# Kernel tuning notes

Measured on AMD Instinct MI355X. Metric: run time of the kernel, lower is better.

## Reference

```python
import jax, jax.numpy as jnp
import numpy as np

B = 8192
D_IN = 10
H = 1900


def _l2norm_cols(w):
    # tf.nn.l2_normalize(w, dim=0): normalize each column, eps 1e-12
    sq = jnp.sum(w * w, axis=0, keepdims=True)
    return w * jax.lax.rsqrt(jnp.maximum(sq, 1e-12))


def setup_inputs() -> dict:
    key = jax.random.key(0)
    ks = jax.random.split(key, 12)
    return {
        "inputs": jax.random.normal(ks[0], (B, D_IN), jnp.float32),
        "c_prev": jax.random.normal(ks[1], (B, H), jnp.float32),
        "h_prev": jax.random.normal(ks[2], (B, H), jnp.float32),
        "wx": jax.random.normal(ks[3], (D_IN, 4 * H), jnp.float32) * 0.1,
        "wh": jax.random.normal(ks[4], (H, 4 * H), jnp.float32) * 0.1,
        "wmx": jax.random.normal(ks[5], (D_IN, H), jnp.float32) * 0.1,
        "wmh": jax.random.normal(ks[6], (H, H), jnp.float32) * 0.1,
        "b": jax.random.normal(ks[7], (4 * H,), jnp.float32) * 0.1,
        "gx": jax.random.uniform(ks[8], (4 * H,), jnp.float32, 0.5, 1.5),
        "gh": jax.random.uniform(ks[9], (4 * H,), jnp.float32, 0.5, 1.5),
        "gmx": jax.random.uniform(ks[10], (H,), jnp.float32, 0.5, 1.5),
        "gmh": jax.random.uniform(ks[11], (H,), jnp.float32, 0.5, 1.5),
    }


def reference(inputs, c_prev, h_prev, wx, wh, wmx, wmh, b, gx, gh, gmx, gmh):
    # weight-normalized weights (per-column l2 norm * gain)
    wx_n = _l2norm_cols(wx) * gx
    wh_n = _l2norm_cols(wh) * gh
    wmx_n = _l2norm_cols(wmx) * gmx
    wmh_n = _l2norm_cols(wmh) * gmh
    # multiplicative state m: [B, H]
    m = (inputs @ wmx_n) * (h_prev @ wmh_n)
    # gate pre-activations z: [B, 4H]
    z = inputs @ wx_n + m @ wh_n + b
    i, f, o, u = jnp.split(z, 4, axis=1)
    i = jax.nn.sigmoid(i)
    f = jax.nn.sigmoid(f)
    o = jax.nn.sigmoid(o)
    u = jnp.tanh(u)
    c = f * c_prev + i * u
    h = o * jnp.tanh(c)
    return (h, c)
```

## Files before the change

### kernel.cpp

```cpp
#include <hip/hip_runtime.h>

typedef unsigned short ushort_t;
typedef short bf16x8 __attribute__((ext_vector_type(8)));
typedef float f32x4 __attribute__((ext_vector_type(4)));

#define H 1900
#define FH 7600
#define BATCH 8192
#define KP 1952
#define NP_A 1920
#define NB 7680
#define BK 32
#define KITERS (KP / BK)

static const size_t OFF_SWX  = 0;
static const size_t OFF_SWH  = 32768;
static const size_t OFF_SWMX = 65536;
static const size_t OFF_SWMH = 73728;
static const size_t OFF_WMXN = 81920;
static const size_t OFF_PART = 163840;
static const size_t OFF_HBF  = 786432;
static const size_t OFF_MEXT = OFF_HBF + 31981568;
static const size_t OFF_WMHT = OFF_MEXT + 31981568;
static const size_t OFF_WHXT = OFF_WMHT + 7495680;

#define PW_X  0
#define PW_H  60800
#define PW_MX 121600
#define PW_MH 136800

__device__ __forceinline__ ushort_t f2bf(float x) {
  unsigned u = __float_as_uint(x);
  return (ushort_t)((u + 0x7fffu + ((u >> 16) & 1u)) >> 16);
}

__device__ __forceinline__ void gl_lds16(const ushort_t* g, ushort_t* lds) {
  __builtin_amdgcn_global_load_lds(
      (const __attribute__((address_space(1))) unsigned int*)(g),
      (__attribute__((address_space(3))) unsigned int*)(lds), 16, 0, 0);
}

__global__ void colsum_partial_kernel(const float* __restrict__ wx, const float* __restrict__ wh,
                                      const float* __restrict__ wmx, const float* __restrict__ wmh,
                                      float* __restrict__ parts) {
  int c = blockIdx.x * 256 + threadIdx.x;
  int y = blockIdx.y, p = blockIdx.z;
  const float* W; int K, N; float* out;
  if (y == 0)      { W = wx;  K = 10;   N = FH; out = parts + PW_X  + (size_t)p * FH; }
  else if (y == 1) { W = wh;  K = 1900; N = FH; out = parts + PW_H  + (size_t)p * FH; }
  else if (y == 2) { W = wmx; K = 10;   N = H;  out = parts + PW_MX + (size_t)p * H;  }
  else             { W = wmh; K = 1900; N = H;  out = parts + PW_MH + (size_t)p * H;  }
  if (c >= N) return;
  int rp = (K + 7) / 8;
  int r0 = p * rp, r1 = r0 + rp; if (r1 > K) r1 = K;
  float s = 0.f;
  for (int r = r0; r < r1; ++r) { float v = W[(size_t)r * N + c]; s += v * v; }
  out[c] = s;
}

__global__ void scales_final_kernel(const float* __restrict__ parts,
                                    const float* __restrict__ gx, const float* __restrict__ gh,
                                    const float* __restrict__ gmx, const float* __restrict__ gmh,
                                    float* __restrict__ s_wx, float* __restrict__ s_wh,
                                    float* __restrict__ s_wmx, float* __restrict__ s_wmh) {
  int c = blockIdx.x * 256 + threadIdx.x;
  int y = blockIdx.y;
  const float* pp; int N; const float* g; float* out;
  if (y == 0)      { pp = parts + PW_X;  N = FH; g = gx;  out = s_wx;  }
  else if (y == 1) { pp = parts + PW_H;  N = FH; g = gh;  out = s_wh;  }
  else if (y == 2) { pp = parts + PW_MX; N = H;  g = gmx; out = s_wmx; }
  else             { pp = parts + PW_MH; N = H;  g = gmh; out = s_wmh; }
  if (c >= N) return;
  float s = 0.f;
  for (int p = 0; p < 8; ++p) s += pp[(size_t)p * N + c];
  out[c] = g[c] * rsqrtf(fmaxf(s, 1e-12f));
}

__global__ void cvt_h_kernel(const float* __restrict__ h_prev, ushort_t* __restrict__ hbf) {
  size_t idx = (size_t)blockIdx.x * 256 + threadIdx.x;
  int row = (int)(idx / KP), col = (int)(idx % KP);
  float v = (col < H) ? h_prev[(size_t)row * H + col] : 0.f;
  hbf[idx] = f2bf(v);
}

__global__ void wmxn_kernel(const float* __restrict__ wmx, const float* __restrict__ s_wmx,
                            float* __restrict__ wmxn) {
  int idx = blockIdx.x * 256 + threadIdx.x;
  int i = idx / NP_A, j = idx - i * NP_A;
  wmxn[idx] = (j < H) ? wmx[i * H + j] * s_wmx[j] : 0.f;
}

__global__ void wmhT_kernel(const float* __restrict__ wmh, const float* __restrict__ s_wmh,
                            ushort_t* __restrict__ wmhT) {
  __shared__ float tile[32][33];
  int n0 = blockIdx.x * 32, k0 = blockIdx.y * 32;
  int tx = threadIdx.x & 31, ty = threadIdx.x >> 5;
#pragma unroll
  for (int it = 0; it < 4; ++it) {
    int k = k0 + ty + it * 8, n = n0 + tx;
    float v = (k < H && n < H) ? wmh[(size_t)k * H + n] : 0.f;
    tile[ty + it * 8][tx] = v;
  }
  __syncthreads();
#pragma unroll
  for (int it = 0; it < 4; ++it) {
    int n = n0 + ty + it * 8, k = k0 + tx;
    float v = tile[tx][ty + it * 8];
    float s = (n < H) ? s_wmh[n] : 0.f;
    wmhT[(size_t)n * KP + k] = f2bf(v * s);
  }
}

__global__ void whxT_kernel(const float* __restrict__ wh, const float* __restrict__ wx,
                            const float* __restrict__ s_wh, const float* __restrict__ s_wx,
                            ushort_t* __restrict__ whxT) {
  __shared__ float tile[32][33];
  int c0 = blockIdx.x * 32, k0 = blockIdx.y * 32;
  int tx = threadIdx.x & 31, ty = threadIdx.x >> 5;
#pragma unroll
  for (int it = 0; it < 4; ++it) {
    int k = k0 + ty + it * 8, c = c0 + tx;
    float v = 0.f;
    if (c < FH) {
      if (k < H) v = wh[(size_t)k * FH + c] * s_wh[c];
      else if (k >= NP_A && k < NP_A + 10) v = wx[(size_t)(k - NP_A) * FH + c] * s_wx[c];
    }
    tile[ty + it * 8][tx] = v;
  }
  __syncthreads();
#pragma unroll
  for (int it = 0; it < 4; ++it) {
    int c = c0 + ty + it * 8, k = k0 + tx;
    if (c < FH) {
      int g = c / H; int j = c - g * H; int n = 4 * j + g;
      whxT[(size_t)n * KP + k] = f2bf(tile[tx][ty + it * 8]);
    }
  }
}

__global__ void mext_tail_kernel(const float* __restrict__ inputs, ushort_t* __restrict__ m_ext) {
  int idx = blockIdx.x * 256 + threadIdx.x;
  int row = idx >> 5, c = idx & 31;
  float v = (c < 10) ? inputs[(size_t)row * 10 + c] : 0.f;
  m_ext[(size_t)row * KP + NP_A + c] = f2bf(v);
}

__global__ void whxT_tail_kernel(ushort_t* __restrict__ whxT) {
  int idx = blockIdx.x * 256 + threadIdx.x;
  whxT[(size_t)FH * KP + idx] = 0;
}

__device__ __forceinline__ void gemm_tile(const ushort_t* __restrict__ Ag,
                                          const ushort_t* __restrict__ Bg,
                                          int m0, int n0,
                                          ushort_t* As, ushort_t* Bs,
                                          f32x4 acc[4][4]) {
  const int tid = threadIdx.x;
  const int lane = tid & 63;
  const int quad = lane >> 4;
  const int lo = lane & 15;
  const int wave = tid >> 6;
  const int wm = (wave & 1) << 6;
  const int wn = (wave >> 1) << 6;
  const int sw = (lo >> 1) & 3;

  const int cr = lane >> 2;
  const int hg = (lane & 3) ^ ((lane >> 3) & 3);
  const int r0 = wave * 16 + cr;
  const int r1 = 64 + wave * 16 + cr;
  const ushort_t* gA0 = Ag + (size_t)(m0 + r0) * KP + hg * 8;
  const ushort_t* gA1 = Ag + (size_t)(m0 + r1) * KP + hg * 8;
  const ushort_t* gB0 = Bg + (size_t)(n0 + r0) * KP + hg * 8;
  const ushort_t* gB1 = Bg + (size_t)(n0 + r1) * KP + hg * 8;
  ushort_t* lA0 = As + (wave * 16) * BK;
  ushort_t* lA1 = As + (64 + wave * 16) * BK;
  ushort_t* lB0 = Bs + (wave * 16) * BK;
  ushort_t* lB1 = Bs + (64 + wave * 16) * BK;

  for (int kt = 0; kt < KITERS; ++kt) {
    __syncthreads();
    gl_lds16(gA0, lA0);
    gl_lds16(gA1, lA1);
    gl_lds16(gB0, lB0);
    gl_lds16(gB1, lB1);
    __syncthreads();
    bf16x8 af[4], bfv[4];
#pragma unroll
    for (int mf = 0; mf < 4; ++mf)
      af[mf] = *(const bf16x8*)(As + (wm + mf * 16 + lo) * BK + ((quad ^ sw) << 3));
#pragma unroll
    for (int nf = 0; nf < 4; ++nf)
      bfv[nf] = *(const bf16x8*)(Bs + (wn + nf * 16 + lo) * BK + ((quad ^ sw) << 3));
#pragma unroll
    for (int mf = 0; mf < 4; ++mf)
#pragma unroll
      for (int nf = 0; nf < 4; ++nf)
        acc[mf][nf] = __builtin_amdgcn_mfma_f32_16x16x32_bf16(af[mf], bfv[nf], acc[mf][nf], 0, 0, 0);
    gA0 += BK; gA1 += BK; gB0 += BK; gB1 += BK;
  }
}

__global__ void __launch_bounds__(256) gemmA_kernel(const ushort_t* __restrict__ hbf,
                                                    const ushort_t* __restrict__ wmhT,
                                                    const float* __restrict__ inputs,
                                                    const float* __restrict__ wmxn,
                                                    ushort_t* __restrict__ m_ext) {
  __shared__ __align__(16) char smem[16384];
  ushort_t* As = (ushort_t*)smem;
  ushort_t* Bs = (ushort_t*)(smem + 8192);
  f32x4 acc[4][4];
  f32x4 zv = {0.f, 0.f, 0.f, 0.f};
#pragma unroll
  for (int a = 0; a < 4; ++a)
#pragma unroll
    for (int bq = 0; bq < 4; ++bq) acc[a][bq] = zv;
  int m0 = blockIdx.x * 128, n0 = blockIdx.y * 128;
  gemm_tile(hbf, wmhT, m0, n0, As, Bs, acc);
  __syncthreads();
  float* inL  = (float*)smem;
  float* wmxL = (float*)(smem + 5120);
  for (int t = threadIdx.x; t < 1280; t += 256) {
    int r = t / 10, i = t - r * 10;
    inL[t] = inputs[(size_t)(m0 + r) * 10 + i];
  }
  for (int t = threadIdx.x; t < 1280; t += 256) {
    int i = t >> 7, c = t & 127;
    wmxL[t] = wmxn[i * NP_A + n0 + c];
  }
  __syncthreads();
  const int lane = threadIdx.x & 63, quad = lane >> 4, lo = lane & 15;
  const int wave = threadIdx.x >> 6, wm = (wave & 1) << 6, wn = (wave >> 1) << 6;
#pragma unroll
  for (int mf = 0; mf < 4; ++mf)
#pragma unroll
    for (int r = 0; r < 4; ++r) {
      int rl = wm + mf * 16 + quad * 4 + r;
      float inrow[10];
#pragma unroll
      for (int i = 0; i < 10; ++i) inrow[i] = inL[rl * 10 + i];
#pragma unroll
      for (int nf = 0; nf < 4; ++nf) {
        int cl = wn + nf * 16 + lo;
        float mx = 0.f;
#pragma unroll
        for (int i = 0; i < 10; ++i) mx += inrow[i] * wmxL[i * 128 + cl];
        float mv = acc[mf][nf][r] * mx;
        m_ext[(size_t)(m0 + rl) * KP + (n0 + cl)] = f2bf(mv);
      }
    }
}

__global__ void __launch_bounds__(256) gemmB_kernel(const ushort_t* __restrict__ mext,
                                                    const ushort_t* __restrict__ whxT,
                                                    const float* __restrict__ bvec,
                                                    const float* __restrict__ c_prev,
                                                    float* __restrict__ hout,
                                                    float* __restrict__ cout) {
  __shared__ __align__(16) char smem[16384];
  ushort_t* As = (ushort_t*)smem;
  ushort_t* Bs = (ushort_t*)(smem + 8192);
  f32x4 acc[4][4];
  f32x4 zv = {0.f, 0.f, 0.f, 0.f};
#pragma unroll
  for (int a = 0; a < 4; ++a)
#pragma unroll
    for (int bq = 0; bq < 4; ++bq) acc[a][bq] = zv;
  int m0 = blockIdx.x * 128, n0 = blockIdx.y * 128;
  gemm_tile(mext, whxT, m0, n0, As, Bs, acc);
  const int lane = threadIdx.x & 63, quad = lane >> 4, lo = lane & 15;
  const int wave = threadIdx.x >> 6, wm = (wave & 1) << 6, wn = (wave >> 1) << 6;
#pragma unroll
  for (int nf = 0; nf < 4; ++nf) {
    int gn = n0 + wn + nf * 16 + lo;
    int j = gn >> 2, g = gn & 3;
    float bias = (j < H) ? bvec[g * H + j] : 0.f;
#pragma unroll
    for (int mf = 0; mf < 4; ++mf)
#pragma unroll
      for (int r = 0; r < 4; ++r) {
        float zs = acc[mf][nf][r] + bias;
        float v1 = __shfl_xor(zs, 1);
        float v2 = __shfl_xor(zs, 2);
        float v3 = __shfl_xor(v1, 2);
        if (g == r && j < H) {
          float zi, zf, zo, zu;
          { int t = 0 ^ g; zi = t == 0 ? zs : t == 1 ? v1 : t == 2 ? v2 : v3; }
          { int t = 1 ^ g; zf = t == 0 ? zs : t == 1 ? v1 : t == 2 ? v2 : v3; }
          { int t = 2 ^ g; zo = t == 0 ? zs : t == 1 ? v1 : t == 2 ? v2 : v3; }
          { int t = 3 ^ g; zu = t == 0 ? zs : t == 1 ? v1 : t == 2 ? v2 : v3; }
          float iv = 1.f / (1.f + __expf(-zi));
          float fv = 1.f / (1.f + __expf(-zf));
          float ov = 1.f / (1.f + __expf(-zo));
          float uv = tanhf(zu);
          int row = m0 + wm + mf * 16 + quad * 4 + r;
          size_t oidx = (size_t)row * H + j;
          float cp = c_prev[oidx];
          float cv = fv * cp + iv * uv;
          hout[oidx] = ov * tanhf(cv);
          cout[oidx] = cv;
        }
      }
  }
}

extern "C" void kernel_launch(void* const* d_in, const int* in_sizes, int n_in,
                              void* d_out, int out_size, void* d_ws, size_t ws_size,
                              hipStream_t stream) {
  const float* inputs = (const float*)d_in[0];
  const float* c_prev = (const float*)d_in[1];
  const float* h_prev = (const float*)d_in[2];
  const float* wx  = (const float*)d_in[3];
  const float* wh  = (const float*)d_in[4];
  const float* wmx = (const float*)d_in[5];
  const float* wmh = (const float*)d_in[6];
  const float* bv  = (const float*)d_in[7];
  const float* gx  = (const float*)d_in[8];
  const float* gh  = (const float*)d_in[9];
  const float* gmx = (const float*)d_in[10];
  const float* gmh = (const float*)d_in[11];

  char* ws = (char*)d_ws;
  float* s_wx  = (float*)(ws + OFF_SWX);
  float* s_wh  = (float*)(ws + OFF_SWH);
  float* s_wmx = (float*)(ws + OFF_SWMX);
  float* s_wmh = (float*)(ws + OFF_SWMH);
  float* wmxn  = (float*)(ws + OFF_WMXN);
  float* parts = (float*)(ws + OFF_PART);
  ushort_t* hbf   = (ushort_t*)(ws + OFF_HBF);
  ushort_t* m_ext = (ushort_t*)(ws + OFF_MEXT);
  ushort_t* wmhT  = (ushort_t*)(ws + OFF_WMHT);
  ushort_t* whxT  = (ushort_t*)(ws + OFF_WHXT);

  float* hout = (float*)d_out;
  float* cout = hout + (size_t)BATCH * H;

  colsum_partial_kernel<<<dim3(30, 4, 8), 256, 0, stream>>>(wx, wh, wmx, wmh, parts);
  scales_final_kernel<<<dim3(30, 4), 256, 0, stream>>>(parts, gx, gh, gmx, gmh,
                                                       s_wx, s_wh, s_wmx, s_wmh);
  cvt_h_kernel<<<62464, 256, 0, stream>>>(h_prev, hbf);
  wmxn_kernel<<<75, 256, 0, stream>>>(wmx, s_wmx, wmxn);
  wmhT_kernel<<<dim3(60, 61), 256, 0, stream>>>(wmh, s_wmh, wmhT);
  whxT_kernel<<<dim3(238, 61), 256, 0, stream>>>(wh, wx, s_wh, s_wx, whxT);
  mext_tail_kernel<<<1024, 256, 0, stream>>>(inputs, m_ext);
  whxT_tail_kernel<<<610, 256, 0, stream>>>(whxT);
  gemmA_kernel<<<dim3(64, 15), 256, 0, stream>>>(hbf, wmhT, inputs, wmxn, m_ext);
  gemmB_kernel<<<dim3(64, 60), 256, 0, stream>>>(m_ext, whxT, bv, c_prev, hout, cout);
}
```

Measured before the change: 1.081 ms.

## Double-buffer LDS tiles in GEMM main loop to overlap loads with MFMA

Splits shared memory into two A/B buffers so the next K-slice is loaded into one buffer while MFMAs run on the other. This cuts the K-loop from two barriers per iteration to one and hides global-to-LDS latency. KITERS is odd, so the loop is unrolled by two with a single tail step. LDS per block doubles to 32 KB, which may reduce occupancy.

```diff
diff --git a/kernel.cpp b/kernel.cpp
--- a/kernel.cpp
+++ b/kernel.cpp
@@ -12,6 +12,7 @@
 #define NB 7680
 #define BK 32
 #define KITERS (KP / BK)
+static_assert(KITERS % 2 == 1, "tail handling assumes odd KITERS");
 
 static const size_t OFF_SWX  = 0;
 static const size_t OFF_SWH  = 32768;
@@ -150,11 +151,45 @@
   whxT[(size_t)FH * KP + idx] = 0;
 }
 
+
+__device__ __forceinline__ void mfma_step(const ushort_t* As, const ushort_t* Bs,
+                                          int wm, int wn, int lo, int quad, int sw,
+                                          f32x4 acc[4][4]) {
+  bf16x8 af[4], bfv[4];
+#pragma unroll
+  for (int mf = 0; mf < 4; ++mf)
+    af[mf] = *(const bf16x8*)(As + (wm + mf * 16 + lo) * BK + ((quad ^ sw) << 3));
+#pragma unroll
+  for (int nf = 0; nf < 4; ++nf)
+    bfv[nf] = *(const bf16x8*)(Bs + (wn + nf * 16 + lo) * BK + ((quad ^ sw) << 3));
+#pragma unroll
+  for (int mf = 0; mf < 4; ++mf)
+#pragma unroll
+    for (int nf = 0; nf < 4; ++nf)
+      acc[mf][nf] = __builtin_amdgcn_mfma_f32_16x16x32_bf16(af[mf], bfv[nf], acc[mf][nf], 0, 0, 0);
+}
+
+__device__ __forceinline__ void gemm_stage(const ushort_t*& gA0, const ushort_t*& gA1,
+                                           const ushort_t*& gB0, const ushort_t*& gB1,
+                                           ushort_t* lA0, ushort_t* lA1,
+                                           ushort_t* lB0, ushort_t* lB1) {
+  gl_lds16(gA0, lA0);
+  gl_lds16(gA1, lA1);
+  gl_lds16(gB0, lB0);
+  gl_lds16(gB1, lB1);
+  gA0 += BK; gA1 += BK; gB0 += BK; gB1 += BK;
+}
+
 __device__ __forceinline__ void gemm_tile(const ushort_t* __restrict__ Ag,
                                           const ushort_t* __restrict__ Bg,
                                           int m0, int n0,
-                                          ushort_t* As, ushort_t* Bs,
+                                          char* smem,
                                           f32x4 acc[4][4]) {
+  ushort_t* As0 = (ushort_t*)(smem);
+  ushort_t* Bs0 = (ushort_t*)(smem + 8192);
+  ushort_t* As1 = (ushort_t*)(smem + 16384);
+  ushort_t* Bs1 = (ushort_t*)(smem + 24576);
+
   const int tid = threadIdx.x;
   const int lane = tid & 63;
   const int quad = lane >> 4;
@@ -172,32 +207,28 @@
   const ushort_t* gA1 = Ag + (size_t)(m0 + r1) * KP + hg * 8;
   const ushort_t* gB0 = Bg + (size_t)(n0 + r0) * KP + hg * 8;
   const ushort_t* gB1 = Bg + (size_t)(n0 + r1) * KP + hg * 8;
-  ushort_t* lA0 = As + (wave * 16) * BK;
-  ushort_t* lA1 = As + (64 + wave * 16) * BK;
-  ushort_t* lB0 = Bs + (wave * 16) * BK;
-  ushort_t* lB1 = Bs + (64 + wave * 16) * BK;
-
-  for (int kt = 0; kt < KITERS; ++kt) {
+  ushort_t* lA0_0 = As0 + (wave * 16) * BK;
+  ushort_t* lA1_0 = As0 + (64 + wave * 16) * BK;
+  ushort_t* lB0_0 = Bs0 + (wave * 16) * BK;
+  ushort_t* lB1_0 = Bs0 + (64 + wave * 16) * BK;
+  ushort_t* lA0_1 = As1 + (wave * 16) * BK;
+  ushort_t* lA1_1 = As1 + (64 + wave * 16) * BK;
+  ushort_t* lB0_1 = Bs1 + (wave * 16) * BK;
+  ushort_t* lB1_1 = Bs1 + (64 + wave * 16) * BK;
+
+  gemm_stage(gA0, gA1, gB0, gB1, lA0_0, lA1_0, lB0_0, lB1_0);
+  __syncthreads();
+
+  for (int kt = 0; kt + 2 < KITERS; kt += 2) {
+    gemm_stage(gA0, gA1, gB0, gB1, lA0_1, lA1_1, lB0_1, lB1_1);
+    mfma_step(As0, Bs0, wm, wn, lo, quad, sw, acc);
     __syncthreads();
-    gl_lds16(gA0, lA0);
-    gl_lds16(gA1, lA1);
-    gl_lds16(gB0, lB0);
-    gl_lds16(gB1, lB1);
+    gemm_stage(gA0, gA1, gB0, gB1, lA0_0, lA1_0, lB0_0, lB1_0);
+    mfma_step(As1, Bs1, wm, wn, lo, quad, sw, acc);
     __syncthreads();
-    bf16x8 af[4], bfv[4];
-#pragma unroll
-    for (int mf = 0; mf < 4; ++mf)
-      af[mf] = *(const bf16x8*)(As + (wm + mf * 16 + lo) * BK + ((quad ^ sw) << 3));
-#pragma unroll
-    for (int nf = 0; nf < 4; ++nf)
-      bfv[nf] = *(const bf16x8*)(Bs + (wn + nf * 16 + lo) * BK + ((quad ^ sw) << 3));
-#pragma unroll
-    for (int mf = 0; mf < 4; ++mf)
-#pragma unroll
-      for (int nf = 0; nf < 4; ++nf)
-        acc[mf][nf] = __builtin_amdgcn_mfma_f32_16x16x32_bf16(af[mf], bfv[nf], acc[mf][nf], 0, 0, 0);
-    gA0 += BK; gA1 += BK; gB0 += BK; gB1 += BK;
-  }
+  }
+  mfma_step(As0, Bs0, wm, wn, lo, quad, sw, acc);
+  __syncthreads();
 }
 
 __global__ void __launch_bounds__(256) gemmA_kernel(const ushort_t* __restrict__ hbf,
@@ -205,9 +236,7 @@
                                                     const float* __restrict__ inputs,
                                                     const float* __restrict__ wmxn,
                                                     ushort_t* __restrict__ m_ext) {
-  __shared__ __align__(16) char smem[16384];
-  ushort_t* As = (ushort_t*)smem;
-  ushort_t* Bs = (ushort_t*)(smem + 8192);
+  __shared__ __align__(16) char smem[32768];
   f32x4 acc[4][4];
   f32x4 zv = {0.f, 0.f, 0.f, 0.f};
 #pragma unroll
@@ -215,8 +244,7 @@
 #pragma unroll
     for (int bq = 0; bq < 4; ++bq) acc[a][bq] = zv;
   int m0 = blockIdx.x * 128, n0 = blockIdx.y * 128;
-  gemm_tile(hbf, wmhT, m0, n0, As, Bs, acc);
-  __syncthreads();
+  gemm_tile(hbf, wmhT, m0, n0, smem, acc);
   float* inL  = (float*)smem;
   float* wmxL = (float*)(smem + 5120);
   for (int t = threadIdx.x; t < 1280; t += 256) {
@@ -256,9 +284,7 @@
                                                     const float* __restrict__ c_prev,
                                                     float* __restrict__ hout,
                                                     float* __restrict__ cout) {
-  __shared__ __align__(16) char smem[16384];
-  ushort_t* As = (ushort_t*)smem;
-  ushort_t* Bs = (ushort_t*)(smem + 8192);
+  __shared__ __align__(16) char smem[32768];
   f32x4 acc[4][4];
   f32x4 zv = {0.f, 0.f, 0.f, 0.f};
 #pragma unroll
@@ -266,7 +292,7 @@
 #pragma unroll
     for (int bq = 0; bq < 4; ++bq) acc[a][bq] = zv;
   int m0 = blockIdx.x * 128, n0 = blockIdx.y * 128;
-  gemm_tile(mext, whxT, m0, n0, As, Bs, acc);
+  gemm_tile(mext, whxT, m0, n0, smem, acc);
   const int lane = threadIdx.x & 63, quad = lane >> 4, lo = lane & 15;
   const int wave = threadIdx.x >> 6, wm = (wave & 1) << 6, wn = (wave >> 1) << 6;
 #pragma unroll
```

After: 1.239 ms. 1.15x slower.

## Replace gate GEMM with 256x256 double-buffered 8-wave pipelined kernel

Applied to the files above, without the earlier changes.

The second GEMM (m_ext × whxT with fused LSTM epilogue) moves from 128x128 tiles with 256 threads to 256x256 tiles with 512 threads. It uses 128KB of dynamic LDS split into two buffers, and global-to-LDS loads for the next K-steps are interleaved with MFMA quarter-tiles. Barriers, setprio and explicit vmcnt waits pace that interleave, and a block-index swizzle groups tiles for L2 reuse. The aim is to raise arithmetic intensity and hide load latency in the dominant GEMM. In exchange it adds heavy register pressure from 128 accumulators per thread and a K tail handled as a separate step, and only one block fits per CU because of the LDS size.

```diff
diff --git a/kernel.cpp b/kernel.cpp
--- a/kernel.cpp
+++ b/kernel.cpp
@@ -12,6 +12,8 @@
 #define NB 7680
 #define BK 32
 #define KITERS (KP / BK)
+
+#define NKT 30
 
 static const size_t OFF_SWX  = 0;
 static const size_t OFF_SWH  = 32768;
@@ -28,6 +30,12 @@
 #define PW_H  60800
 #define PW_MX 121600
 #define PW_MH 136800
+
+#define BAR() __builtin_amdgcn_s_barrier()
+#define PRIO1 __builtin_amdgcn_s_setprio(1)
+#define PRIO0 __builtin_amdgcn_s_setprio(0)
+#define WAIT_LGKM0 asm volatile("s_waitcnt lgkmcnt(0)" ::: "memory")
+#define WAIT_VM(N) asm volatile("s_waitcnt vmcnt(" #N ")" ::: "memory")
 
 __device__ __forceinline__ ushort_t f2bf(float x) {
   unsigned u = __float_as_uint(x);
@@ -150,11 +158,11 @@
   whxT[(size_t)FH * KP + idx] = 0;
 }
 
-__device__ __forceinline__ void gemm_tile(const ushort_t* __restrict__ Ag,
-                                          const ushort_t* __restrict__ Bg,
-                                          int m0, int n0,
-                                          ushort_t* As, ushort_t* Bs,
-                                          f32x4 acc[4][4]) {
+__device__ __forceinline__ void gemm_tile128(const ushort_t* __restrict__ Ag,
+                                             const ushort_t* __restrict__ Bg,
+                                             int m0, int n0,
+                                             ushort_t* As, ushort_t* Bs,
+                                             f32x4 acc[4][4]) {
   const int tid = threadIdx.x;
   const int lane = tid & 63;
   const int quad = lane >> 4;
@@ -215,7 +223,7 @@
 #pragma unroll
     for (int bq = 0; bq < 4; ++bq) acc[a][bq] = zv;
   int m0 = blockIdx.x * 128, n0 = blockIdx.y * 128;
-  gemm_tile(hbf, wmhT, m0, n0, As, Bs, acc);
+  gemm_tile128(hbf, wmhT, m0, n0, As, Bs, acc);
   __syncthreads();
   float* inL  = (float*)smem;
   float* wmxL = (float*)(smem + 5120);
@@ -250,32 +258,182 @@
     }
 }
 
-__global__ void __launch_bounds__(256) gemmB_kernel(const ushort_t* __restrict__ mext,
-                                                    const ushort_t* __restrict__ whxT,
-                                                    const float* __restrict__ bvec,
-                                                    const float* __restrict__ c_prev,
-                                                    float* __restrict__ hout,
-                                                    float* __restrict__ cout) {
-  __shared__ __align__(16) char smem[16384];
-  ushort_t* As = (ushort_t*)smem;
-  ushort_t* Bs = (ushort_t*)(smem + 8192);
-  f32x4 acc[4][4];
+
+__device__ __forceinline__ void stage_half(const ushort_t* __restrict__ G, int Rg, int kb,
+                                           ushort_t* L, int tid) {
+  const int wave = tid >> 6;
+#pragma unroll
+  for (int q = 0; q < 2; ++q) {
+    const int idx = q * 512 + tid;
+    const int r = idx >> 3, s = idx & 7;
+    const int gs = s ^ (r & 7);
+    gl_lds16(G + (size_t)(Rg + r) * KP + kb + gs * 8,
+             L + (size_t)(q * 512 + wave * 64) * 8);
+  }
+}
+
+__device__ __forceinline__ void read_Ahalf(const ushort_t* A, int wmL, int lo, int mh,
+                                           int sw0, int sw1, bf16x8 af[8]) {
+#pragma unroll
+  for (int mf = 0; mf < 4; ++mf) {
+    const ushort_t* p = A + ((wmL + mh * 64 + mf * 16 + lo) << 6);
+    af[mf * 2 + 0] = *(const bf16x8*)(p + sw0);
+    af[mf * 2 + 1] = *(const bf16x8*)(p + sw1);
+  }
+}
+
+__device__ __forceinline__ void read_Bhalf(const ushort_t* B, int wnL, int lo, int nh,
+                                           int sw0, int sw1, bf16x8 bf[4]) {
+#pragma unroll
+  for (int nf = 0; nf < 2; ++nf) {
+    const ushort_t* p = B + ((wnL + nh * 32 + nf * 16 + lo) << 6);
+    bf[nf * 2 + 0] = *(const bf16x8*)(p + sw0);
+    bf[nf * 2 + 1] = *(const bf16x8*)(p + sw1);
+  }
+}
+
+__device__ __forceinline__ void mfma_quad(const bf16x8 af[8], const bf16x8 bf[4],
+                                          f32x4 acc[8][4], int mh, int nh) {
+#pragma unroll
+  for (int mf = 0; mf < 4; ++mf)
+#pragma unroll
+    for (int nf = 0; nf < 2; ++nf) {
+      f32x4 c = acc[mh * 4 + mf][nh * 2 + nf];
+      c = __builtin_amdgcn_mfma_f32_16x16x32_bf16(af[mf * 2 + 0], bf[nf * 2 + 0], c, 0, 0, 0);
+      c = __builtin_amdgcn_mfma_f32_16x16x32_bf16(af[mf * 2 + 1], bf[nf * 2 + 1], c, 0, 0, 0);
+      acc[mh * 4 + mf][nh * 2 + nf] = c;
+    }
+}
+
+template <int MODE>
+__device__ __forceinline__ void b8_iter(const ushort_t* __restrict__ Ag,
+                                        const ushort_t* __restrict__ Bg,
+                                        int m0, int n0, int T,
+                                        ushort_t* Acur, ushort_t* Bcur,
+                                        ushort_t* Anxt, ushort_t* Bnxt,
+                                        int tid, int lo, int wmL, int wnL,
+                                        int sw0, int sw1, f32x4 acc[8][4]) {
+  bf16x8 af[8], b0f[4], b1f[4];
+  read_Ahalf(Acur, wmL, lo, 0, sw0, sw1, af);
+  read_Bhalf(Bcur, wnL, lo, 0, sw0, sw1, b0f);
+  if (MODE <= 1) stage_half(Ag, m0 + 128, (T + 1) * 64, Anxt + 8192, tid);
+  BAR(); WAIT_LGKM0;
+  PRIO1; mfma_quad(af, b0f, acc, 0, 0); PRIO0;
+  BAR();
+  read_Bhalf(Bcur, wnL, lo, 1, sw0, sw1, b1f);
+  BAR(); WAIT_LGKM0;
+  PRIO1; mfma_quad(af, b1f, acc, 0, 1); PRIO0;
+  BAR();
+  read_Ahalf(Acur, wmL, lo, 1, sw0, sw1, af);
+  if (MODE == 0) stage_half(Bg, n0, (T + 2) * 64, Bcur, tid);
+  BAR(); WAIT_LGKM0;
+  PRIO1; mfma_quad(af, b1f, acc, 1, 1); PRIO0;
+  BAR();
+  if (MODE == 0) {
+    stage_half(Ag, m0, (T + 2) * 64, Acur, tid);
+    stage_half(Bg, n0 + 128, (T + 2) * 64, Bcur + 8192, tid);
+    WAIT_VM(6);
+  } else if (MODE == 1) {
+    WAIT_VM(0);
+  }
+  BAR();
+  PRIO1; mfma_quad(af, b0f, acc, 1, 0); PRIO0;
+  BAR();
+}
+
+__global__ void __launch_bounds__(512, 2)
+gemmB8_kernel(const ushort_t* __restrict__ mext, const ushort_t* __restrict__ whxT,
+              const float* __restrict__ bvec, const float* __restrict__ c_prev,
+              float* __restrict__ hout, float* __restrict__ cout) {
+  extern __shared__ __align__(16) char smem[];
+  ushort_t* As0 = (ushort_t*)smem;
+  ushort_t* Bs0 = (ushort_t*)(smem + 32768);
+  ushort_t* As1 = (ushort_t*)(smem + 65536);
+  ushort_t* Bs1 = (ushort_t*)(smem + 98304);
+
+  const int tid = threadIdx.x;
+  const int lane = tid & 63;
+  const int lo = lane & 15, quad = lane >> 4;
+  const int wave = tid >> 6;
+  const int wmL = (wave & 1) << 7;
+  const int wnL = (wave >> 1) << 6;
+  const int sw0 = ((quad ^ (lo & 7)) << 3);
+  const int sw1 = (((4 | quad) ^ (lo & 7)) << 3);
+
+  int bid = blockIdx.x;
+  int swz = (bid & 7) * 120 + (bid >> 3);
+  int mt = swz & 31, nt = swz >> 5;
+  int m0 = mt << 8, n0 = nt << 8;
+
+  f32x4 acc[8][4];
   f32x4 zv = {0.f, 0.f, 0.f, 0.f};
 #pragma unroll
-  for (int a = 0; a < 4; ++a)
+  for (int a = 0; a < 8; ++a)
 #pragma unroll
     for (int bq = 0; bq < 4; ++bq) acc[a][bq] = zv;
-  int m0 = blockIdx.x * 128, n0 = blockIdx.y * 128;
-  gemm_tile(mext, whxT, m0, n0, As, Bs, acc);
-  const int lane = threadIdx.x & 63, quad = lane >> 4, lo = lane & 15;
-  const int wave = threadIdx.x >> 6, wm = (wave & 1) << 6, wn = (wave >> 1) << 6;
+
+  const ushort_t* Ag = mext;
+  const ushort_t* Bg = whxT;
+
+  stage_half(Ag, m0,       0,  As0,        tid);
+  stage_half(Bg, n0,       0,  Bs0,        tid);
+  stage_half(Ag, m0 + 128, 0,  As0 + 8192, tid);
+  stage_half(Bg, n0 + 128, 0,  Bs0 + 8192, tid);
+  stage_half(Bg, n0,       64, Bs1,        tid);
+  stage_half(Ag, m0,       64, As1,        tid);
+  stage_half(Bg, n0 + 128, 64, Bs1 + 8192, tid);
+  WAIT_VM(6);
+  BAR();
+
+  for (int T = 0; T < NKT - 2; T += 2) {
+    b8_iter<0>(Ag, Bg, m0, n0, T,     As0, Bs0, As1, Bs1, tid, lo, wmL, wnL, sw0, sw1, acc);
+    b8_iter<0>(Ag, Bg, m0, n0, T + 1, As1, Bs1, As0, Bs0, tid, lo, wmL, wnL, sw0, sw1, acc);
+  }
+  b8_iter<1>(Ag, Bg, m0, n0, NKT - 2, As0, Bs0, As1, Bs1, tid, lo, wmL, wnL, sw0, sw1, acc);
+  b8_iter<2>(Ag, Bg, m0, n0, NKT - 1, As1, Bs1, As0, Bs0, tid, lo, wmL, wnL, sw0, sw1, acc);
+
+  {
+    const int wavei = tid >> 6;
+#pragma unroll
+    for (int q = 0; q < 2; ++q) {
+      const int idx = q * 512 + tid;
+      const int r = idx >> 2, s = idx & 3;
+      const int gs = s ^ (r & 3);
+      gl_lds16(Ag + (size_t)(m0 + r) * KP + 1920 + gs * 8,
+               As0 + (size_t)(q * 512 + wavei * 64) * 8);
+    }
+#pragma unroll
+    for (int q = 0; q < 2; ++q) {
+      const int idx = q * 512 + tid;
+      const int r = idx >> 2, s = idx & 3;
+      const int gs = s ^ (r & 3);
+      gl_lds16(Bg + (size_t)(n0 + r) * KP + 1920 + gs * 8,
+               Bs0 + (size_t)(q * 512 + wavei * 64) * 8);
+    }
+    WAIT_VM(0);
+    BAR();
+    const int swt = ((quad ^ (lo & 3)) << 3);
+    bf16x8 a2[8], b2[4];
+#pragma unroll
+    for (int mf = 0; mf < 8; ++mf)
+      a2[mf] = *(const bf16x8*)(As0 + ((wmL + mf * 16 + lo) << 5) + swt);
+#pragma unroll
+    for (int nf = 0; nf < 4; ++nf)
+      b2[nf] = *(const bf16x8*)(Bs0 + ((wnL + nf * 16 + lo) << 5) + swt);
+#pragma unroll
+    for (int mf = 0; mf < 8; ++mf)
+#pragma unroll
+      for (int nf = 0; nf < 4; ++nf)
+        acc[mf][nf] = __builtin_amdgcn_mfma_f32_16x16x32_bf16(a2[mf], b2[nf], acc[mf][nf], 0, 0, 0);
+  }
+
 #pragma unroll
   for (int nf = 0; nf < 4; ++nf) {
-    int gn = n0 + wn + nf * 16 + lo;
+    int gn = n0 + wnL + nf * 16 + lo;
     int j = gn >> 2, g = gn & 3;
     float bias = (j < H) ? bvec[g * H + j] : 0.f;
 #pragma unroll
-    for (int mf = 0; mf < 4; ++mf)
+    for (int mf = 0; mf < 8; ++mf)
 #pragma unroll
       for (int r = 0; r < 4; ++r) {
         float zs = acc[mf][nf][r] + bias;
@@ -292,7 +450,7 @@
           float fv = 1.f / (1.f + __expf(-zf));
           float ov = 1.f / (1.f + __expf(-zo));
           float uv = tanhf(zu);
-          int row = m0 + wm + mf * 16 + quad * 4 + r;
+          int row = m0 + wmL + mf * 16 + quad * 4 + r;
           size_t oidx = (size_t)row * H + j;
           float cp = c_prev[oidx];
           float cv = fv * cp + iv * uv;
@@ -334,6 +492,13 @@
   float* hout = (float*)d_out;
   float* cout = hout + (size_t)BATCH * H;
 
+  static bool attr_set = false;
+  if (!attr_set) {
+    hipFuncSetAttribute(reinterpret_cast<const void*>(&gemmB8_kernel),
+                        hipFuncAttributeMaxDynamicSharedMemorySize, 131072);
+    attr_set = true;
+  }
+
   colsum_partial_kernel<<<dim3(30, 4, 8), 256, 0, stream>>>(wx, wh, wmx, wmh, parts);
   scales_final_kernel<<<dim3(30, 4), 256, 0, stream>>>(parts, gx, gh, gmx, gmh,
                                                        s_wx, s_wh, s_wmx, s_wmh);
@@ -344,5 +509,5 @@
   mext_tail_kernel<<<1024, 256, 0, stream>>>(inputs, m_ext);
   whxT_tail_kernel<<<610, 256, 0, stream>>>(whxT);
   gemmA_kernel<<<dim3(64, 15), 256, 0, stream>>>(hbf, wmhT, inputs, wmxn, m_ext);
-  gemmB_kernel<<<dim3(64, 60), 256, 0, stream>>>(m_ext, whxT, bv, c_prev, hout, cout);
-}
+  gemmB8_kernel<<<dim3(960), 512, 131072, stream>>>(m_ext, whxT, bv, c_prev, hout, cout);
+}
```

After: 1.093 ms. About the same (+1.1%).

## Tile m_ext/whxT into contiguous slabs and triple-buffer gemmB with XCD-aware block mapping

Applied to the files above, without the earlier changes.

Stores m_ext and the transposed gate weights in a 128x32 slab-tiled layout, so each K-step loads one contiguous 8 KB chunk per operand. The main gemm is rewritten as a triple-buffered LDS pipeline that prefetches two slabs ahead using direct global-to-LDS loads, partial vmcnt waits and raw barriers, and raises wave priority around the MFMA block. It also remaps block IDs so each XCD works on a contiguous group of M tiles, aiming for better L2 reuse. The costs are triple the LDS per block (48 KB) and a fragile manual waitcnt schedule.

```diff
diff --git a/kernel.cpp b/kernel.cpp
--- a/kernel.cpp
+++ b/kernel.cpp
@@ -9,9 +9,12 @@
 #define BATCH 8192
 #define KP 1952
 #define NP_A 1920
-#define NB 7680
 #define BK 32
 #define KITERS (KP / BK)
+
+#define NSLAB 61
+#define SLAB_U 4096
+#define PANEL_U 249856
 
 static const size_t OFF_SWX  = 0;
 static const size_t OFF_SWH  = 32768;
@@ -29,6 +32,11 @@
 #define PW_MX 121600
 #define PW_MH 136800
 
+#define BAR() __builtin_amdgcn_s_barrier()
+#define PRIO1 __builtin_amdgcn_s_setprio(1)
+#define PRIO0 __builtin_amdgcn_s_setprio(0)
+#define WAIT_VM(N) asm volatile("s_waitcnt vmcnt(" #N ")" ::: "memory")
+
 __device__ __forceinline__ ushort_t f2bf(float x) {
   unsigned u = __float_as_uint(x);
   return (ushort_t)((u + 0x7fffu + ((u >> 16) & 1u)) >> 16);
@@ -38,6 +46,11 @@
   __builtin_amdgcn_global_load_lds(
       (const __attribute__((address_space(1))) unsigned int*)(g),
       (__attribute__((address_space(3))) unsigned int*)(lds), 16, 0, 0);
+}
+
+__device__ __forceinline__ size_t tiled_addr(int row, int col) {
+  return (size_t)(row >> 7) * PANEL_U + (size_t)(col >> 5) * SLAB_U +
+         (size_t)(row & 127) * 32 + (col & 31);
 }
 
 __global__ void colsum_partial_kernel(const float* __restrict__ wx, const float* __restrict__ wh,
@@ -133,7 +146,7 @@
     int c = c0 + ty + it * 8, k = k0 + tx;
     if (c < FH) {
       int g = c / H; int j = c - g * H; int n = 4 * j + g;
-      whxT[(size_t)n * KP + k] = f2bf(tile[tx][ty + it * 8]);
+      whxT[tiled_addr(n, k)] = f2bf(tile[tx][ty + it * 8]);
     }
   }
 }
@@ -142,19 +155,20 @@
   int idx = blockIdx.x * 256 + threadIdx.x;
   int row = idx >> 5, c = idx & 31;
   float v = (c < 10) ? inputs[(size_t)row * 10 + c] : 0.f;
-  m_ext[(size_t)row * KP + NP_A + c] = f2bf(v);
+  m_ext[tiled_addr(row, 1920 + c)] = f2bf(v);
 }
 
 __global__ void whxT_tail_kernel(ushort_t* __restrict__ whxT) {
   int idx = blockIdx.x * 256 + threadIdx.x;
-  whxT[(size_t)FH * KP + idx] = 0;
-}
-
-__device__ __forceinline__ void gemm_tile(const ushort_t* __restrict__ Ag,
-                                          const ushort_t* __restrict__ Bg,
-                                          int m0, int n0,
-                                          ushort_t* As, ushort_t* Bs,
-                                          f32x4 acc[4][4]) {
+  int n = 7600 + idx / 1952, k = idx % 1952;
+  whxT[tiled_addr(n, k)] = 0;
+}
+
+__device__ __forceinline__ void gemm_tile128(const ushort_t* __restrict__ Ag,
+                                             const ushort_t* __restrict__ Bg,
+                                             int m0, int n0,
+                                             ushort_t* As, ushort_t* Bs,
+                                             f32x4 acc[4][4]) {
   const int tid = threadIdx.x;
   const int lane = tid & 63;
   const int quad = lane >> 4;
@@ -215,7 +229,7 @@
 #pragma unroll
     for (int bq = 0; bq < 4; ++bq) acc[a][bq] = zv;
   int m0 = blockIdx.x * 128, n0 = blockIdx.y * 128;
-  gemm_tile(hbf, wmhT, m0, n0, As, Bs, acc);
+  gemm_tile128(hbf, wmhT, m0, n0, As, Bs, acc);
   __syncthreads();
   float* inL  = (float*)smem;
   float* wmxL = (float*)(smem + 5120);
@@ -245,35 +259,112 @@
 #pragma unroll
         for (int i = 0; i < 10; ++i) mx += inrow[i] * wmxL[i * 128 + cl];
         float mv = acc[mf][nf][r] * mx;
-        m_ext[(size_t)(m0 + rl) * KP + (n0 + cl)] = f2bf(mv);
+        m_ext[tiled_addr(m0 + rl, n0 + cl)] = f2bf(mv);
       }
     }
 }
 
-__global__ void __launch_bounds__(256) gemmB_kernel(const ushort_t* __restrict__ mext,
-                                                    const ushort_t* __restrict__ whxT,
-                                                    const float* __restrict__ bvec,
-                                                    const float* __restrict__ c_prev,
-                                                    float* __restrict__ hout,
-                                                    float* __restrict__ cout) {
-  __shared__ __align__(16) char smem[16384];
-  ushort_t* As = (ushort_t*)smem;
-  ushort_t* Bs = (ushort_t*)(smem + 8192);
+
+__device__ __forceinline__ void stage_slab(const ushort_t* __restrict__ Gp, int slab,
+                                           ushort_t* L, int tid) {
+  const int wave = tid >> 6;
+#pragma unroll
+  for (int q = 0; q < 2; ++q) {
+    const int idx = q * 256 + tid;
+    const int r = idx >> 2, s = idx & 3;
+    const int gs = s ^ (r & 3);
+    gl_lds16(Gp + (size_t)slab * SLAB_U + r * 32 + gs * 8,
+             L + (size_t)(q * 256 + wave * 64) * 8);
+  }
+}
+
+template <int MODE>
+__device__ __forceinline__ void b5_step(const ushort_t* __restrict__ Ap,
+                                        const ushort_t* __restrict__ Bp, int t,
+                                        ushort_t* Acur, ushort_t* Bcur,
+                                        ushort_t* Astg, ushort_t* Bstg,
+                                        int tid, int lo, int quad, int wm, int wn,
+                                        f32x4 acc[4][4]) {
+  if (MODE == 0) {
+    stage_slab(Ap, t + 2, Astg, tid);
+    stage_slab(Bp, t + 2, Bstg, tid);
+  }
+  const int k0 = (quad ^ (lo & 3)) << 3;
+  bf16x8 af[4], bfv[4];
+#pragma unroll
+  for (int mf = 0; mf < 4; ++mf)
+    af[mf] = *(const bf16x8*)(Acur + ((wm + mf * 16 + lo) << 5) + k0);
+#pragma unroll
+  for (int nf = 0; nf < 4; ++nf)
+    bfv[nf] = *(const bf16x8*)(Bcur + ((wn + nf * 16 + lo) << 5) + k0);
+  PRIO1;
+#pragma unroll
+  for (int mf = 0; mf < 4; ++mf)
+#pragma unroll
+    for (int nf = 0; nf < 4; ++nf)
+      acc[mf][nf] = __builtin_amdgcn_mfma_f32_16x16x32_bf16(af[mf], bfv[nf], acc[mf][nf], 0, 0, 0);
+  PRIO0;
+  if (MODE == 0) { WAIT_VM(4); BAR(); }
+  else if (MODE == 1) { WAIT_VM(0); BAR(); }
+}
+
+__global__ void __launch_bounds__(256, 3)
+gemmB5_kernel(const ushort_t* __restrict__ mext, const ushort_t* __restrict__ whxT,
+              const float* __restrict__ bvec, const float* __restrict__ c_prev,
+              float* __restrict__ hout, float* __restrict__ cout) {
+  __shared__ __align__(16) char smem[49152];
+  ushort_t* As[3] = {(ushort_t*)smem, (ushort_t*)(smem + 16384), (ushort_t*)(smem + 32768)};
+  ushort_t* Bs[3] = {(ushort_t*)(smem + 8192), (ushort_t*)(smem + 24576),
+                     (ushort_t*)(smem + 40960)};
+
+  const int tid = threadIdx.x;
+  const int lane = tid & 63;
+  const int lo = lane & 15, quad = lane >> 4;
+  const int wave = tid >> 6;
+  const int wm = (wave & 1) << 6;
+  const int wn = (wave >> 1) << 6;
+
+  int bid = blockIdx.x;
+  int xcd = bid & 7, jj = bid >> 3;
+  int mt = (xcd << 3) | (jj & 7);
+  int nt = jj >> 3;
+  int m0 = mt << 7, n0 = nt << 7;
+
   f32x4 acc[4][4];
   f32x4 zv = {0.f, 0.f, 0.f, 0.f};
 #pragma unroll
   for (int a = 0; a < 4; ++a)
 #pragma unroll
     for (int bq = 0; bq < 4; ++bq) acc[a][bq] = zv;
-  int m0 = blockIdx.x * 128, n0 = blockIdx.y * 128;
-  gemm_tile(mext, whxT, m0, n0, As, Bs, acc);
-  const int lane = threadIdx.x & 63, quad = lane >> 4, lo = lane & 15;
-  const int wave = threadIdx.x >> 6, wm = (wave & 1) << 6, wn = (wave >> 1) << 6;
+
+  const ushort_t* Ap = mext + (size_t)mt * PANEL_U;
+  const ushort_t* Bp = whxT + (size_t)nt * PANEL_U;
+
+  stage_slab(Ap, 0, As[0], tid);
+  stage_slab(Bp, 0, Bs[0], tid);
+  stage_slab(Ap, 1, As[1], tid);
+  stage_slab(Bp, 1, Bs[1], tid);
+  WAIT_VM(4);
+  BAR();
+
+  for (int t = 0; t < 54; t += 3) {
+    b5_step<0>(Ap, Bp, t,     As[0], Bs[0], As[2], Bs[2], tid, lo, quad, wm, wn, acc);
+    b5_step<0>(Ap, Bp, t + 1, As[1], Bs[1], As[0], Bs[0], tid, lo, quad, wm, wn, acc);
+    b5_step<0>(Ap, Bp, t + 2, As[2], Bs[2], As[1], Bs[1], tid, lo, quad, wm, wn, acc);
+  }
+  b5_step<0>(Ap, Bp, 54, As[0], Bs[0], As[2], Bs[2], tid, lo, quad, wm, wn, acc);
+  b5_step<0>(Ap, Bp, 55, As[1], Bs[1], As[0], Bs[0], tid, lo, quad, wm, wn, acc);
+  b5_step<0>(Ap, Bp, 56, As[2], Bs[2], As[1], Bs[1], tid, lo, quad, wm, wn, acc);
+  b5_step<0>(Ap, Bp, 57, As[0], Bs[0], As[2], Bs[2], tid, lo, quad, wm, wn, acc);
+  b5_step<0>(Ap, Bp, 58, As[1], Bs[1], As[0], Bs[0], tid, lo, quad, wm, wn, acc);
+  b5_step<1>(Ap, Bp, 59, As[2], Bs[2], nullptr, nullptr, tid, lo, quad, wm, wn, acc);
+  b5_step<2>(Ap, Bp, 60, As[0], Bs[0], nullptr, nullptr, tid, lo, quad, wm, wn, acc);
+
 #pragma unroll
   for (int nf = 0; nf < 4; ++nf) {
     int gn = n0 + wn + nf * 16 + lo;
-    int j = gn >> 2, g = gn & 3;
-    float bias = (j < H) ? bvec[g * H + j] : 0.f;
+    int j2 = gn >> 2, g = gn & 3;
+    float bias = (j2 < H) ? bvec[g * H + j2] : 0.f;
 #pragma unroll
     for (int mf = 0; mf < 4; ++mf)
 #pragma unroll
@@ -282,7 +373,7 @@
         float v1 = __shfl_xor(zs, 1);
         float v2 = __shfl_xor(zs, 2);
         float v3 = __shfl_xor(v1, 2);
-        if (g == r && j < H) {
+        if (g == r && j2 < H) {
           float zi, zf, zo, zu;
           { int t = 0 ^ g; zi = t == 0 ? zs : t == 1 ? v1 : t == 2 ? v2 : v3; }
           { int t = 1 ^ g; zf = t == 0 ? zs : t == 1 ? v1 : t == 2 ? v2 : v3; }
@@ -293,7 +384,7 @@
           float ov = 1.f / (1.f + __expf(-zo));
           float uv = tanhf(zu);
           int row = m0 + wm + mf * 16 + quad * 4 + r;
-          size_t oidx = (size_t)row * H + j;
+          size_t oidx = (size_t)row * H + j2;
           float cp = c_prev[oidx];
           float cv = fv * cp + iv * uv;
           hout[oidx] = ov * tanhf(cv);
@@ -344,5 +435,5 @@
   mext_tail_kernel<<<1024, 256, 0, stream>>>(inputs, m_ext);
   whxT_tail_kernel<<<610, 256, 0, stream>>>(whxT);
   gemmA_kernel<<<dim3(64, 15), 256, 0, stream>>>(hbf, wmhT, inputs, wmxn, m_ext);
-  gemmB_kernel<<<dim3(64, 60), 256, 0, stream>>>(m_ext, whxT, bv, c_prev, hout, cout);
-}
+  gemmB5_kernel<<<3840, 256, 0, stream>>>(m_ext, whxT, bv, c_prev, hout, cout);
+}
```

After: 950.1 us. 1.14x faster.
